# Kernel optimization log

Hardware: AMD Instinct MI355X
Metric: run time of the kernel (lower is better)

Reference implementation:

```python
import jax, jax.numpy as jnp
import numpy as np

OUT, IN = 11008, 4096
B, S = 8, 32


def setup_inputs() -> dict:
    key = jax.random.key(0)
    k_x, k_w, k_s, k_b = jax.random.split(key, 4)
    x = jax.random.normal(k_x, (B, S, IN), dtype=jnp.float32).astype(jnp.float16)
    # int8 weight storage (symmetric quant range [-128, 127])
    w_int8 = jax.random.randint(k_w, (OUT, IN), -128, 128, dtype=jnp.int32).astype(jnp.int8)
    # per-output-channel scale, small positive values typical of int8 quant
    scale = jax.random.uniform(k_s, (OUT,), dtype=jnp.float32) * 0.01 + 1e-4
    bias = (jax.random.normal(k_b, (OUT,), dtype=jnp.float32) * 0.02).astype(jnp.float16)
    return {"x": x, "w_int8": w_int8, "scale": scale, "bias": bias}


def reference(x, w_int8, scale, bias):
    # w_fp[o, i] = int8_weight[o, i] * scale[o]   (on-the-fly dequant)
    w = w_int8.astype(jnp.float32) * scale[:, None]          # [OUT, IN] fp32
    # F.linear: out = x @ w.T + bias, computed in fp32
    out = jnp.einsum('bsi,oi->bso', x.astype(jnp.float32), w) + bias.astype(jnp.float32)
    return out.astype(x.dtype)                                # cast back to x.dtype (fp16)
```

## Files before the change

### kernel.cpp

```cpp
#include <hip/hip_runtime.h>
#include <hip/hip_bf16.h>
#include <stdint.h>

typedef __attribute__((ext_vector_type(8))) __bf16 bf16x8;
typedef __attribute__((ext_vector_type(4))) float f32x4;

constexpr int K_DIM = 4096;
constexpr int N_DIM = 11008;
constexpr int M_DIM = 256;
constexpr int TM = 256;
constexpr int TN = 64;
constexpr int BK = 64;
constexpr int NT = 512;
constexpr int KT_ALL = K_DIM / BK;
constexpr int KSPLIT = 3;

__device__ __forceinline__ void gload_lds16(const __bf16* gptr, __bf16* lptr) {
  __builtin_amdgcn_global_load_lds(
      (const __attribute__((address_space(1))) uint32_t*)gptr,
      (__attribute__((address_space(3))) uint32_t*)lptr, 16, 0, 0);
}

__device__ __forceinline__ bf16x8 cvt8(const float4 u0, const float4 u1) {
  bf16x8 v;
  v[0] = (__bf16)u0.x; v[1] = (__bf16)u0.y; v[2] = (__bf16)u0.z; v[3] = (__bf16)u0.w;
  v[4] = (__bf16)u1.x; v[5] = (__bf16)u1.y; v[6] = (__bf16)u1.z; v[7] = (__bf16)u1.w;
  return v;
}

__global__ void cvt_x_kernel(const float* __restrict__ x, __bf16* __restrict__ ws) {
  const int i = (blockIdx.x * 256 + threadIdx.x) * 8;
  const float4 u0 = ((const float4*)(x + i))[0];
  const float4 u1 = ((const float4*)(x + i))[1];
  *(bf16x8*)(ws + i) = cvt8(u0, u1);
}

template<bool USE_WS>
__global__ __launch_bounds__(NT, 4) void int8_linear_kernel(
    const float* __restrict__ x,
    const __bf16* __restrict__ xws,
    const int*   __restrict__ w,
    const float* __restrict__ scale,
    const float* __restrict__ bias,
    float*       __restrict__ out)
{
  __shared__ __bf16 As[2][TM * BK];
  __shared__ __bf16 Wsh[2][TN * BK];

  const int tid  = threadIdx.x;
  const int lane = tid & 63;
  const int wv   = tid >> 6;
  const int quad = lane >> 4;
  const int l16  = lane & 15;
  const int wm   = wv >> 1;
  const int wn   = wv & 1;
  const int m_base = wm * 64;
  const int n_base = blockIdx.x * TN;
  const int kc     = blockIdx.y;

  const int t0 = (kc * KT_ALL) / KSPLIT;
  const int t1 = ((kc + 1) * KT_ALL) / KSPLIT;
  const int ntile = t1 - t0;
  const int k0 = t0 * BK;

  const int wrow   = tid >> 3;
  const int wchunk = tid & 7;
  const int wslot  = wchunk ^ (wrow & 7);
  const int* wptr = w + (int64_t)(n_base + wrow) * K_DIM + k0 + wchunk * 8;

  f32x4 acc[4][2];
#pragma unroll
  for (int i = 0; i < 4; ++i)
#pragma unroll
    for (int j = 0; j < 2; ++j) acc[i][j] = (f32x4){0.f, 0.f, 0.f, 0.f};

  int4 wrA[2], wrB[2];
  auto wload = [&](int t, int4* wr) {
    const int4* p = (const int4*)(wptr + t * BK);
    wr[0] = p[0]; wr[1] = p[1];
  };
  auto commitW = [&](const int4* wr, __bf16* wbuf) {
    bf16x8 v;
    v[0] = (__bf16)(float)wr[0].x; v[1] = (__bf16)(float)wr[0].y;
    v[2] = (__bf16)(float)wr[0].z; v[3] = (__bf16)(float)wr[0].w;
    v[4] = (__bf16)(float)wr[1].x; v[5] = (__bf16)(float)wr[1].y;
    v[6] = (__bf16)(float)wr[1].z; v[7] = (__bf16)(float)wr[1].w;
    *(bf16x8*)(wbuf + wrow * BK + wslot * 8) = v;
  };
  auto a_stage = [&](int t, __bf16* abuf) {
    if (USE_WS) {
#pragma unroll
      for (int j = 0; j < 4; ++j) {
        const int c = j * 512 + tid;
        const int row = c >> 3;
        const int k8 = (c & 7) ^ (row & 7);
        gload_lds16(xws + (int64_t)row * K_DIM + (t0 + t) * BK + k8 * 8, abuf + c * 8);
      }
    } else {
#pragma unroll
      for (int j = 0; j < 4; ++j) {
        const int c = j * 512 + tid;
        const int row = c >> 3;
        const int k8 = c & 7;
        const float* s = x + (int64_t)row * K_DIM + (t0 + t) * BK + k8 * 8;
        const bf16x8 v = cvt8(((const float4*)s)[0], ((const float4*)s)[1]);
        const int slot = k8 ^ (row & 7);
        *(bf16x8*)(abuf + row * BK + slot * 8) = v;
      }
    }
  };
  auto compute = [&](const __bf16* abuf, const __bf16* wbuf) {
#pragma unroll
    for (int ks = 0; ks < 2; ++ks) {
      bf16x8 a[4], b[2];
#pragma unroll
      for (int mi = 0; mi < 4; ++mi) {
        const int m = m_base + mi * 16 + l16;
        const int slot = (ks * 4 + quad) ^ (m & 7);
        a[mi] = *(const bf16x8*)(abuf + m * BK + slot * 8);
      }
#pragma unroll
      for (int ni = 0; ni < 2; ++ni) {
        const int n = wn * 32 + ni * 16 + l16;
        const int slot = (ks * 4 + quad) ^ (n & 7);
        b[ni] = *(const bf16x8*)(wbuf + n * BK + slot * 8);
      }
#pragma unroll
      for (int mi = 0; mi < 4; ++mi)
#pragma unroll
        for (int ni = 0; ni < 2; ++ni)
          acc[mi][ni] = __builtin_amdgcn_mfma_f32_16x16x32_bf16(
              a[mi], b[ni], acc[mi][ni], 0, 0, 0);
    }
  };

  wload(0, wrA);
  __builtin_amdgcn_sched_barrier(0);
  a_stage(0, As[0]);
  __builtin_amdgcn_sched_barrier(0);
  wload(1, wrB);
  commitW(wrA, Wsh[0]);
  asm volatile("s_waitcnt vmcnt(2)" ::: "memory");
  asm volatile("s_waitcnt lgkmcnt(0)" ::: "memory");
  __builtin_amdgcn_sched_barrier(0);
  __builtin_amdgcn_s_barrier();
  __builtin_amdgcn_sched_barrier(0);

  for (int t = 0; t < ntile; t += 2) {
    {
      const bool hA = (t + 1 < ntile);
      const bool hW = (t + 2 < ntile);
      if (hA) a_stage(t + 1, As[1]);
      __builtin_amdgcn_sched_barrier(0);
      if (hW) wload(t + 2, wrA);
      if (hA) commitW(wrB, Wsh[1]);
      compute(As[0], Wsh[0]);
      if (hA) {
        if (hW) asm volatile("s_waitcnt vmcnt(2)" ::: "memory");
        else    asm volatile("s_waitcnt vmcnt(0)" ::: "memory");
        asm volatile("s_waitcnt lgkmcnt(0)" ::: "memory");
        __builtin_amdgcn_sched_barrier(0);
        __builtin_amdgcn_s_barrier();
        __builtin_amdgcn_sched_barrier(0);
      }
    }
    if (t + 1 < ntile) {
      const bool hA = (t + 2 < ntile);
      const bool hW = (t + 3 < ntile);
      if (hA) a_stage(t + 2, As[0]);
      __builtin_amdgcn_sched_barrier(0);
      if (hW) wload(t + 3, wrB);
      if (hA) commitW(wrA, Wsh[0]);
      compute(As[1], Wsh[1]);
      if (hA) {
        if (hW) asm volatile("s_waitcnt vmcnt(2)" ::: "memory");
        else    asm volatile("s_waitcnt vmcnt(0)" ::: "memory");
        asm volatile("s_waitcnt lgkmcnt(0)" ::: "memory");
        __builtin_amdgcn_sched_barrier(0);
        __builtin_amdgcn_s_barrier();
        __builtin_amdgcn_sched_barrier(0);
      }
    }
  }

#pragma unroll
  for (int ni = 0; ni < 2; ++ni) {
    const int col = n_base + wn * 32 + ni * 16 + l16;
    const float sc = scale[col];
    const float bi = (kc == 0) ? bias[col] : 0.0f;
#pragma unroll
    for (int mi = 0; mi < 4; ++mi) {
      const int row0 = m_base + mi * 16 + quad * 4;
#pragma unroll
      for (int r = 0; r < 4; ++r)
        unsafeAtomicAdd(out + (int64_t)(row0 + r) * N_DIM + col,
                        acc[mi][ni][r] * sc + bi);
    }
  }
}

extern "C" void kernel_launch(void* const* d_in, const int* in_sizes, int n_in,
                              void* d_out, int out_size, void* d_ws, size_t ws_size,
                              hipStream_t stream) {
  const float* x     = (const float*)d_in[0];
  const int*   w     = (const int*)d_in[1];
  const float* scale = (const float*)d_in[2];
  const float* bias  = (const float*)d_in[3];
  float* out = (float*)d_out;

  __bf16* xws = (__bf16*)d_ws;
  const bool use_ws = ws_size >= (size_t)M_DIM * K_DIM * sizeof(__bf16);

  hipMemsetAsync(out, 0, (size_t)M_DIM * N_DIM * sizeof(float), stream);

  dim3 grid(N_DIM / TN, KSPLIT), block(NT);
  if (use_ws) {
    cvt_x_kernel<<<M_DIM * K_DIM / (256 * 8), 256, 0, stream>>>(x, xws);
    int8_linear_kernel<true><<<grid, block, 0, stream>>>(x, xws, w, scale, bias, out);
  } else {
    int8_linear_kernel<false><<<grid, block, 0, stream>>>(x, xws, w, scale, bias, out);
  }
}
```

Baseline: 306.4 us.

## Pre-convert weights to bf16 in workspace and load via direct-to-LDS

Adds a separate kernel that converts the int32-stored weights to bf16 in the workspace, then stages both A and W tiles into LDS with global_load_lds. The main loop is simplified to a single-stage prefetch with __syncthreads instead of the hand-scheduled register double buffering. This removes per-tile weight conversion from the GEMM but adds a full extra pass over the weight matrix (read int32, write bf16, reread bf16) on every call.

```diff
diff --git a/kernel.cpp b/kernel.cpp
--- a/kernel.cpp
+++ b/kernel.cpp
@@ -21,10 +21,18 @@
       (__attribute__((address_space(3))) uint32_t*)lptr, 16, 0, 0);
 }
 
-__device__ __forceinline__ bf16x8 cvt8(const float4 u0, const float4 u1) {
+__device__ __forceinline__ bf16x8 cvt8f(const float4 u0, const float4 u1) {
   bf16x8 v;
   v[0] = (__bf16)u0.x; v[1] = (__bf16)u0.y; v[2] = (__bf16)u0.z; v[3] = (__bf16)u0.w;
   v[4] = (__bf16)u1.x; v[5] = (__bf16)u1.y; v[6] = (__bf16)u1.z; v[7] = (__bf16)u1.w;
+  return v;
+}
+__device__ __forceinline__ bf16x8 cvt8i(const int4 a, const int4 b) {
+  bf16x8 v;
+  v[0] = (__bf16)(float)a.x; v[1] = (__bf16)(float)a.y;
+  v[2] = (__bf16)(float)a.z; v[3] = (__bf16)(float)a.w;
+  v[4] = (__bf16)(float)b.x; v[5] = (__bf16)(float)b.y;
+  v[6] = (__bf16)(float)b.z; v[7] = (__bf16)(float)b.w;
   return v;
 }
 
@@ -32,14 +40,22 @@
   const int i = (blockIdx.x * 256 + threadIdx.x) * 8;
   const float4 u0 = ((const float4*)(x + i))[0];
   const float4 u1 = ((const float4*)(x + i))[1];
-  *(bf16x8*)(ws + i) = cvt8(u0, u1);
+  *(bf16x8*)(ws + i) = cvt8f(u0, u1);
 }
 
-template<bool USE_WS>
+__global__ void cvt_w_kernel(const int* __restrict__ w, __bf16* __restrict__ wbf) {
+  const size_t i = ((size_t)blockIdx.x * 256 + threadIdx.x) * 8;
+  const int4 a = ((const int4*)(w + i))[0];
+  const int4 b = ((const int4*)(w + i))[1];
+  *(bf16x8*)(wbf + i) = cvt8i(a, b);
+}
+
+template<bool A_WS, bool W_WS>
 __global__ __launch_bounds__(NT, 4) void int8_linear_kernel(
     const float* __restrict__ x,
     const __bf16* __restrict__ xws,
     const int*   __restrict__ w,
+    const __bf16* __restrict__ wbf,
     const float* __restrict__ scale,
     const float* __restrict__ bias,
     float*       __restrict__ out)
@@ -52,21 +68,14 @@
   const int wv   = tid >> 6;
   const int quad = lane >> 4;
   const int l16  = lane & 15;
-  const int wm   = wv >> 1;
-  const int wn   = wv & 1;
-  const int m_base = wm * 64;
+  const int m_base = (wv >> 1) * 64;
+  const int wn     = wv & 1;
   const int n_base = blockIdx.x * TN;
   const int kc     = blockIdx.y;
 
   const int t0 = (kc * KT_ALL) / KSPLIT;
   const int t1 = ((kc + 1) * KT_ALL) / KSPLIT;
   const int ntile = t1 - t0;
-  const int k0 = t0 * BK;
-
-  const int wrow   = tid >> 3;
-  const int wchunk = tid & 7;
-  const int wslot  = wchunk ^ (wrow & 7);
-  const int* wptr = w + (int64_t)(n_base + wrow) * K_DIM + k0 + wchunk * 8;
 
   f32x4 acc[4][2];
 #pragma unroll
@@ -74,27 +83,15 @@
 #pragma unroll
     for (int j = 0; j < 2; ++j) acc[i][j] = (f32x4){0.f, 0.f, 0.f, 0.f};
 
-  int4 wrA[2], wrB[2];
-  auto wload = [&](int t, int4* wr) {
-    const int4* p = (const int4*)(wptr + t * BK);
-    wr[0] = p[0]; wr[1] = p[1];
-  };
-  auto commitW = [&](const int4* wr, __bf16* wbuf) {
-    bf16x8 v;
-    v[0] = (__bf16)(float)wr[0].x; v[1] = (__bf16)(float)wr[0].y;
-    v[2] = (__bf16)(float)wr[0].z; v[3] = (__bf16)(float)wr[0].w;
-    v[4] = (__bf16)(float)wr[1].x; v[5] = (__bf16)(float)wr[1].y;
-    v[6] = (__bf16)(float)wr[1].z; v[7] = (__bf16)(float)wr[1].w;
-    *(bf16x8*)(wbuf + wrow * BK + wslot * 8) = v;
-  };
-  auto a_stage = [&](int t, __bf16* abuf) {
-    if (USE_WS) {
+  auto stage = [&](int t, int buf) {
+    const int kt = t0 + t;
+    if (A_WS) {
 #pragma unroll
       for (int j = 0; j < 4; ++j) {
         const int c = j * 512 + tid;
         const int row = c >> 3;
         const int k8 = (c & 7) ^ (row & 7);
-        gload_lds16(xws + (int64_t)row * K_DIM + (t0 + t) * BK + k8 * 8, abuf + c * 8);
+        gload_lds16(xws + (int64_t)row * K_DIM + kt * BK + k8 * 8, As[buf] + c * 8);
       }
     } else {
 #pragma unroll
@@ -102,11 +99,21 @@
         const int c = j * 512 + tid;
         const int row = c >> 3;
         const int k8 = c & 7;
-        const float* s = x + (int64_t)row * K_DIM + (t0 + t) * BK + k8 * 8;
-        const bf16x8 v = cvt8(((const float4*)s)[0], ((const float4*)s)[1]);
-        const int slot = k8 ^ (row & 7);
-        *(bf16x8*)(abuf + row * BK + slot * 8) = v;
+        const float* s = x + (int64_t)row * K_DIM + kt * BK + k8 * 8;
+        const bf16x8 v = cvt8f(((const float4*)s)[0], ((const float4*)s)[1]);
+        *(bf16x8*)(As[buf] + row * BK + (k8 ^ (row & 7)) * 8) = v;
       }
+    }
+    const int row = tid >> 3;
+    const int k8l = tid & 7;
+    if (W_WS) {
+      const int k8 = k8l ^ (row & 7);
+      gload_lds16(wbf + (int64_t)(n_base + row) * K_DIM + kt * BK + k8 * 8,
+                  Wsh[buf] + tid * 8);
+    } else {
+      const int4* p = (const int4*)(w + (int64_t)(n_base + row) * K_DIM + kt * BK + k8l * 8);
+      const bf16x8 v = cvt8i(p[0], p[1]);
+      *(bf16x8*)(Wsh[buf] + row * BK + (k8l ^ (row & 7)) * 8) = v;
     }
   };
   auto compute = [&](const __bf16* abuf, const __bf16* wbuf) {
@@ -134,53 +141,12 @@
     }
   };
 
-  wload(0, wrA);
-  __builtin_amdgcn_sched_barrier(0);
-  a_stage(0, As[0]);
-  __builtin_amdgcn_sched_barrier(0);
-  wload(1, wrB);
-  commitW(wrA, Wsh[0]);
-  asm volatile("s_waitcnt vmcnt(2)" ::: "memory");
-  asm volatile("s_waitcnt lgkmcnt(0)" ::: "memory");
-  __builtin_amdgcn_sched_barrier(0);
-  __builtin_amdgcn_s_barrier();
-  __builtin_amdgcn_sched_barrier(0);
-
-  for (int t = 0; t < ntile; t += 2) {
-    {
-      const bool hA = (t + 1 < ntile);
-      const bool hW = (t + 2 < ntile);
-      if (hA) a_stage(t + 1, As[1]);
-      __builtin_amdgcn_sched_barrier(0);
-      if (hW) wload(t + 2, wrA);
-      if (hA) commitW(wrB, Wsh[1]);
-      compute(As[0], Wsh[0]);
-      if (hA) {
-        if (hW) asm volatile("s_waitcnt vmcnt(2)" ::: "memory");
-        else    asm volatile("s_waitcnt vmcnt(0)" ::: "memory");
-        asm volatile("s_waitcnt lgkmcnt(0)" ::: "memory");
-        __builtin_amdgcn_sched_barrier(0);
-        __builtin_amdgcn_s_barrier();
-        __builtin_amdgcn_sched_barrier(0);
-      }
-    }
-    if (t + 1 < ntile) {
-      const bool hA = (t + 2 < ntile);
-      const bool hW = (t + 3 < ntile);
-      if (hA) a_stage(t + 2, As[0]);
-      __builtin_amdgcn_sched_barrier(0);
-      if (hW) wload(t + 3, wrB);
-      if (hA) commitW(wrA, Wsh[0]);
-      compute(As[1], Wsh[1]);
-      if (hA) {
-        if (hW) asm volatile("s_waitcnt vmcnt(2)" ::: "memory");
-        else    asm volatile("s_waitcnt vmcnt(0)" ::: "memory");
-        asm volatile("s_waitcnt lgkmcnt(0)" ::: "memory");
-        __builtin_amdgcn_sched_barrier(0);
-        __builtin_amdgcn_s_barrier();
-        __builtin_amdgcn_sched_barrier(0);
-      }
-    }
+  stage(0, 0);
+  __syncthreads();
+  for (int t = 0; t < ntile; ++t) {
+    if (t + 1 < ntile) stage(t + 1, (t + 1) & 1);
+    compute(As[t & 1], Wsh[t & 1]);
+    __syncthreads();
   }
 
 #pragma unroll
@@ -208,16 +174,25 @@
   const float* bias  = (const float*)d_in[3];
   float* out = (float*)d_out;
 
+  const size_t xws_bytes = (size_t)M_DIM * K_DIM * sizeof(__bf16);
+  const size_t wbf_bytes = (size_t)N_DIM * K_DIM * sizeof(__bf16);
   __bf16* xws = (__bf16*)d_ws;
-  const bool use_ws = ws_size >= (size_t)M_DIM * K_DIM * sizeof(__bf16);
+  __bf16* wbf = (__bf16*)((char*)d_ws + xws_bytes);
 
   hipMemsetAsync(out, 0, (size_t)M_DIM * N_DIM * sizeof(float), stream);
 
   dim3 grid(N_DIM / TN, KSPLIT), block(NT);
-  if (use_ws) {
-    cvt_x_kernel<<<M_DIM * K_DIM / (256 * 8), 256, 0, stream>>>(x, xws);
-    int8_linear_kernel<true><<<grid, block, 0, stream>>>(x, xws, w, scale, bias, out);
+  if (ws_size >= xws_bytes + wbf_bytes) {
+    cvt_x_kernel<<<M_DIM * K_DIM / 2048, 256, 0, stream>>>(x, xws);
+    cvt_w_kernel<<<(int)(((size_t)N_DIM * K_DIM) / 2048), 256, 0, stream>>>(w, wbf);
+    int8_linear_kernel<true, true><<<grid, block, 0, stream>>>(
+        x, xws, w, wbf, scale, bias, out);
+  } else if (ws_size >= xws_bytes) {
+    cvt_x_kernel<<<M_DIM * K_DIM / 2048, 256, 0, stream>>>(x, xws);
+    int8_linear_kernel<true, false><<<grid, block, 0, stream>>>(
+        x, xws, w, wbf, scale, bias, out);
   } else {
-    int8_linear_kernel<false><<<grid, block, 0, stream>>>(x, xws, w, scale, bias, out);
+    int8_linear_kernel<false, false><<<grid, block, 0, stream>>>(
+        x, xws, w, wbf, scale, bias, out);
   }
 }
```

New measurement: 339.9 us. +10.9%, slower.
